# Optimization experiments

Measured on AMD Instinct MI355X. Metric: run time of the kernel, lower is better.

The kernel has to match this reference:

```python
import jax, jax.numpy as jnp
import numpy as np

B, Q, S, D, H, F = 16, 8, 4096, 2048, 16, 128  # batch, new tokens, past kv, d_state, heads, head_dim
W_SCALE = 0.02  # keep projections well-conditioned for stable softmax


def setup_inputs() -> dict:
    key = jax.random.key(0)
    ks = jax.random.split(key, 8)
    return {
        "x": jax.random.normal(ks[0], (B, Q, D), jnp.float32),
        "cache_k": jax.random.normal(ks[1], (B, S, H, F), jnp.float32),
        "cache_v": jax.random.normal(ks[2], (B, S, H, F), jnp.float32),
        "wq": jax.random.normal(ks[3], (D, H, F), jnp.float32) * W_SCALE,
        "bq": jnp.zeros((H, F), jnp.float32),
        "wk": jax.random.normal(ks[4], (D, H, F), jnp.float32) * W_SCALE,
        "bk": jnp.zeros((H, F), jnp.float32),
        "wv": jax.random.normal(ks[5], (D, H, F), jnp.float32) * W_SCALE,
        "bv": jnp.zeros((H, F), jnp.float32),
        "wo": jax.random.normal(ks[6], (H, F, D), jnp.float32) * W_SCALE,
        "bo": jnp.zeros((D,), jnp.float32),
    }


def reference(x, cache_k, cache_v, wq, bq, wk, bk, wv, bv, wo, bo):
    # QKV projections: DenseGeneral(features=(H, F), axis=-1)
    q = jnp.einsum("bqd,dhf->bqhf", x, wq) + bq          # [B,Q,H,F]
    k_new = jnp.einsum("bqd,dhf->bqhf", x, wk) + bk      # [B,Q,H,F]
    v_new = jnp.einsum("bqd,dhf->bqhf", x, wv) + bv
    # concat-based KV cache growth along the sequence axis (axis=1)
    k = jnp.concatenate([cache_k, k_new], axis=1)        # [B,S+Q,H,F]
    v = jnp.concatenate([cache_v, v_new], axis=1)
    # full dot-product attention over the whole cache (mask=None on decode path)
    scale = 1.0 / jnp.sqrt(jnp.asarray(F, q.dtype))
    scores = jnp.einsum("bqhf,bkhf->bhqk", q, k) * scale  # [B,H,Q,S+Q]
    probs = jax.nn.softmax(scores, axis=-1)
    attn = jnp.einsum("bhqk,bkhf->bhqf", probs, v)        # [B,H,Q,F]
    # output projection: DenseGeneral(features=D, axis=(-3,-1)) contracts (H, F)
    out = jnp.einsum("bhqf,hfd->bqd", attn, wo) + bo      # [B,Q,D]
    return (out, k, v)
```

## Files before the change

kernel.cpp:

```cpp
#include <hip/hip_runtime.h>
#include <hip/hip_bf16.h>

constexpr int Bc = 16;
constexpr int Qc = 8;
constexpr int Sc = 4096;
constexpr int Dc = 2048;
constexpr int Hc = 16;
constexpr int Fc = 128;
constexpr int SP = Sc + Qc;
constexpr int Mr = Bc * Qc;
constexpr int NCHUNK = 9;
constexpr int CHUNK = 512;
constexpr float SCALE = 0.08838834764831845f;
constexpr int GKS = 8;
constexpr int GKC = Dc / GKS;

typedef float floatx4 __attribute__((ext_vector_type(4)));

__device__ __forceinline__ float4 nt_load4(const float* p) {
    floatx4 r = __builtin_nontemporal_load(reinterpret_cast<const floatx4*>(p));
    return make_float4(r.x, r.y, r.z, r.w);
}
__device__ __forceinline__ void nt_store4(float* p, float4 v) {
    floatx4 r; r.x = v.x; r.y = v.y; r.z = v.z; r.w = v.w;
    __builtin_nontemporal_store(r, reinterpret_cast<floatx4*>(p));
}

__global__ __launch_bounds__(256)
void gemm_ksplit(const float* __restrict__ A, const float* __restrict__ W0,
                 const float* __restrict__ W1, const float* __restrict__ W2,
                 float* __restrict__ part)
{
    const int ntile = blockIdx.x;
    const int mat   = blockIdx.y;
    const int kz    = blockIdx.z;
    const float* __restrict__ W = (mat == 0) ? W0 : ((mat == 1) ? W1 : W2);
    const int t  = threadIdx.x;
    const int tx = t & 15, ty = t >> 4;
    const int r0 = ty * 8, c0 = tx * 8;
    const int ncol0 = ntile * 128;

    __shared__ float a_s[128][17];
    __shared__ float w_s[16][128];

    float acc[8][8] = {};

    const int kbase = kz * GKC;
    for (int k0 = kbase; k0 < kbase + GKC; k0 += 16) {
        {
            const int kk = t & 15, r = t >> 4;
            #pragma unroll
            for (int i = 0; i < 8; i++)
                a_s[r + i * 16][kk] = A[(size_t)(r + i * 16) * Dc + k0 + kk];
        }
        {
            const int nn = t & 127, ks_ = t >> 7;
            #pragma unroll
            for (int i = 0; i < 8; i++)
                w_s[ks_ + i * 2][nn] = W[(size_t)(k0 + ks_ + i * 2) * 2048 + ncol0 + nn];
        }
        __syncthreads();
        #pragma unroll
        for (int kk = 0; kk < 16; kk++) {
            float av[8], wv[8];
            #pragma unroll
            for (int i = 0; i < 8; i++) av[i] = a_s[r0 + i][kk];
            #pragma unroll
            for (int j = 0; j < 8; j++) wv[j] = w_s[kk][c0 + j];
            #pragma unroll
            for (int i = 0; i < 8; i++)
                #pragma unroll
                for (int j = 0; j < 8; j++)
                    acc[i][j] += av[i] * wv[j];
        }
        __syncthreads();
    }
    float* __restrict__ dst = part + (size_t)(mat * GKS + kz) * Mr * 2048;
    #pragma unroll
    for (int i = 0; i < 8; i++)
        #pragma unroll
        for (int j = 0; j < 8; j++)
            dst[(size_t)(r0 + i) * 2048 + ncol0 + c0 + j] = acc[i][j];
}

__global__ __launch_bounds__(256)
void reduce_qkv(const float* __restrict__ part, const float* __restrict__ bq,
                const float* __restrict__ bk, const float* __restrict__ bv,
                float* __restrict__ q_ws, float* __restrict__ out_k, float* __restrict__ out_v)
{
    const int mat = blockIdx.y;
    const int e = blockIdx.x * 256 + threadIdx.x;
    const int m = e >> 11, n = e & 2047;
    const float* __restrict__ p = part + (size_t)mat * GKS * (Mr * 2048);
    float s = 0.f;
    #pragma unroll
    for (int ks = 0; ks < GKS; ks++) s += p[(size_t)ks * (Mr * 2048) + e];
    const int b = m >> 3, qi = m & 7;
    if (mat == 0)      { s += bq[n]; q_ws[e] = s; }
    else if (mat == 1) { s += bk[n]; out_k[((size_t)(b * SP + Sc + qi)) * 2048 + n] = s; }
    else               { s += bv[n]; out_v[((size_t)(b * SP + Sc + qi)) * 2048 + n] = s; }
}

template<bool TAIL, int LEN>
__global__ __launch_bounds__(256, 3)
void attn_fused(const float* __restrict__ cache_k, const float* __restrict__ cache_v,
                const float* __restrict__ q_ws,
                float* __restrict__ out_k, float* __restrict__ out_v,
                float* __restrict__ part_acc, float* __restrict__ part_l)
{
    const int c = TAIL ? 8 : blockIdx.x;
    const int h = blockIdx.y;
    const int b = blockIdx.z;
    const int t = threadIdx.x;
    const int w = t >> 6;
    const int lane = t & 63;
    const int half = lane >> 5;
    const int fl = lane & 31;
    const int s0 = c * CHUNK;

    constexpr int kpw = LEN / 4;
    constexpr int pairs = LEN / 8;

    __shared__ float wacc[4][Qc][Fc];
    __shared__ float l_w[4][Qc];

    float4 qreg[Qc];
    #pragma unroll
    for (int qi = 0; qi < Qc; qi++) {
        float4 qv = *reinterpret_cast<const float4*>(
            &q_ws[((size_t)(b * Qc + qi)) * Dc + h * Fc + fl * 4]);
        qv.x *= SCALE; qv.y *= SCALE; qv.z *= SCALE; qv.w *= SCALE;
        qreg[qi] = qv;
    }

    float4 acc[Qc];
    float lsum[Qc];
    #pragma unroll
    for (int i = 0; i < Qc; i++) { acc[i] = make_float4(0, 0, 0, 0); lsum[i] = 0.f; }

    #pragma unroll 4
    for (int j = 0; j < pairs; j++) {
        const int kl = w * kpw + 2 * j + half;
        const int key = s0 + kl;
        const size_t outoff = (((size_t)b * SP + key) * Hc + h) * Fc + fl * 4;
        float4 kv, vv;
        if (!TAIL) {
            const size_t coff = (((size_t)b * Sc + key) * Hc + h) * Fc + fl * 4;
            kv = nt_load4(&cache_k[coff]);
            vv = nt_load4(&cache_v[coff]);
            nt_store4(&out_k[outoff], kv);
            nt_store4(&out_v[outoff], vv);
        } else {
            kv = *reinterpret_cast<const float4*>(&out_k[outoff]);
            vv = *reinterpret_cast<const float4*>(&out_v[outoff]);
        }
        #pragma unroll
        for (int qi = 0; qi < Qc; qi++) {
            float p = kv.x * qreg[qi].x + kv.y * qreg[qi].y
                    + kv.z * qreg[qi].z + kv.w * qreg[qi].w;
            p += __shfl_xor(p, 1, 64);
            p += __shfl_xor(p, 2, 64);
            p += __shfl_xor(p, 4, 64);
            p += __shfl_xor(p, 8, 64);
            p += __shfl_xor(p, 16, 64);
            p = __expf(p);
            lsum[qi] += p;
            acc[qi].x += p * vv.x; acc[qi].y += p * vv.y;
            acc[qi].z += p * vv.z; acc[qi].w += p * vv.w;
        }
    }

    #pragma unroll
    for (int qi = 0; qi < Qc; qi++) {
        acc[qi].x += __shfl_xor(acc[qi].x, 32, 64);
        acc[qi].y += __shfl_xor(acc[qi].y, 32, 64);
        acc[qi].z += __shfl_xor(acc[qi].z, 32, 64);
        acc[qi].w += __shfl_xor(acc[qi].w, 32, 64);
        lsum[qi]  += __shfl_xor(lsum[qi], 32, 64);
    }
    if (half == 0) {
        #pragma unroll
        for (int qi = 0; qi < Qc; qi++)
            *reinterpret_cast<float4*>(&wacc[w][qi][fl * 4]) = acc[qi];
    }
    if (lane == 0) {
        #pragma unroll
        for (int qi = 0; qi < Qc; qi++) l_w[w][qi] = lsum[qi];
    }
    __syncthreads();

    {
        const int qi = t >> 5, f4 = (t & 31) * 4;
        float4 s_ = make_float4(0, 0, 0, 0);
        #pragma unroll
        for (int ww = 0; ww < 4; ww++) {
            const float4 a = *reinterpret_cast<const float4*>(&wacc[ww][qi][f4]);
            s_.x += a.x; s_.y += a.y; s_.z += a.z; s_.w += a.w;
        }
        const size_t idx = (size_t)(b * Hc + h) * NCHUNK + c;
        *reinterpret_cast<float4*>(&part_acc[(idx * Qc + qi) * Fc + f4]) = s_;
        if ((t & 31) == 0)
            part_l[idx * Qc + qi] = l_w[0][qi] + l_w[1][qi] + l_w[2][qi] + l_w[3][qi];
    }
}

__global__ __launch_bounds__(256)
void attn_combine(const float* __restrict__ part_acc, const float* __restrict__ part_l,
                  float* __restrict__ attn_ws)
{
    const int bh = blockIdx.x;
    const int b = bh >> 4, h = bh & 15;
    const int t = threadIdx.x;
    const int qi = t >> 5, f4 = (t & 31) * 4;
    const size_t base = (size_t)bh * NCHUNK;

    float lg = 0.f;
    #pragma unroll
    for (int c = 0; c < NCHUNK; c++) lg += part_l[(base + c) * Qc + qi];
    float4 s_ = make_float4(0, 0, 0, 0);
    #pragma unroll
    for (int c = 0; c < NCHUNK; c++) {
        const float4 a = *reinterpret_cast<const float4*>(
            &part_acc[((base + c) * Qc + qi) * Fc + f4]);
        s_.x += a.x; s_.y += a.y; s_.z += a.z; s_.w += a.w;
    }
    const float inv = 1.0f / lg;
    const float4 o = make_float4(s_.x * inv, s_.y * inv, s_.z * inv, s_.w * inv);
    *reinterpret_cast<float4*>(&attn_ws[((size_t)(b * Qc + qi)) * Dc + h * Fc + f4]) = o;
}

__global__ __launch_bounds__(256)
void reduce_o(const float* __restrict__ part, const float* __restrict__ bo,
              float* __restrict__ out)
{
    const int e = blockIdx.x * 256 + threadIdx.x;
    const int n = e & 2047;
    float s = 0.f;
    #pragma unroll
    for (int ks = 0; ks < GKS; ks++) s += part[(size_t)ks * (Mr * 2048) + e];
    out[e] = s + bo[n];
}

extern "C" void kernel_launch(void* const* d_in, const int* in_sizes, int n_in,
                              void* d_out, int out_size, void* d_ws, size_t ws_size,
                              hipStream_t stream)
{
    (void)in_sizes; (void)n_in; (void)out_size; (void)ws_size;
    const float* x       = (const float*)d_in[0];
    const float* cache_k = (const float*)d_in[1];
    const float* cache_v = (const float*)d_in[2];
    const float* wq      = (const float*)d_in[3];
    const float* bq      = (const float*)d_in[4];
    const float* wk      = (const float*)d_in[5];
    const float* bk      = (const float*)d_in[6];
    const float* wv      = (const float*)d_in[7];
    const float* bv      = (const float*)d_in[8];
    const float* wo      = (const float*)d_in[9];
    const float* bo      = (const float*)d_in[10];

    float* out   = (float*)d_out;
    float* out_k = out + (size_t)Mr * Dc;
    float* out_v = out_k + (size_t)Bc * SP * Hc * Fc;

    float* ws       = (float*)d_ws;
    float* q_ws     = ws;
    float* attn_ws  = ws + 262144;
    float* part_l   = ws + 524288;
    float* part_acc = part_l + 18432;
    float* gemm_part = part_acc + 2359296;

    gemm_ksplit<<<dim3(16, 3, GKS), 256, 0, stream>>>(x, wq, wk, wv, gemm_part);
    reduce_qkv<<<dim3(1024, 3), 256, 0, stream>>>(gemm_part, bq, bk, bv, q_ws, out_k, out_v);
    attn_fused<false, CHUNK><<<dim3(8, Hc, Bc), 256, 0, stream>>>(
        cache_k, cache_v, q_ws, out_k, out_v, part_acc, part_l);
    attn_fused<true, 8><<<dim3(1, Hc, Bc), 256, 0, stream>>>(
        cache_k, cache_v, q_ws, out_k, out_v, part_acc, part_l);
    attn_combine<<<dim3(Bc * Hc), 256, 0, stream>>>(part_acc, part_l, attn_ws);
    gemm_ksplit<<<dim3(16, 1, GKS), 256, 0, stream>>>(attn_ws, wo, wo, wo, gemm_part);
    reduce_o<<<dim3(1024), 256, 0, stream>>>(gemm_part, bo, out);
}
```

Before: 537.0 us.

## Split attention into 256-key chunks, fold tail into last chunk, vectorize reductions

Halves the attention chunk size to 256 keys (16 chunks) and reorders the grid so heads vary fastest, which gives more blocks and raises the occupancy hint to 4. The separate tail launch is removed: the last chunk now also handles the 8 new tokens. The exponential uses exp2 with log2e folded into the query scale. The two bias-and-reduce kernels now work on float4, and part_acc reuses the gemm_part workspace. The cost is more partials for the combine step and a runtime branch inside the attention kernel.

```diff
diff --git a/kernel.cpp b/kernel.cpp
--- a/kernel.cpp
+++ b/kernel.cpp
@@ -9,9 +9,11 @@
 constexpr int Fc = 128;
 constexpr int SP = Sc + Qc;
 constexpr int Mr = Bc * Qc;
-constexpr int NCHUNK = 9;
-constexpr int CHUNK = 512;
+constexpr int CHUNK = 256;
+constexpr int NCHUNK = 16;
 constexpr float SCALE = 0.08838834764831845f;
+constexpr float LOG2E = 1.4426950408889634f;
+constexpr float QSCALE = SCALE * LOG2E;
 constexpr int GKS = 8;
 constexpr int GKC = Dc / GKS;
 
@@ -89,27 +91,40 @@
                 float* __restrict__ q_ws, float* __restrict__ out_k, float* __restrict__ out_v)
 {
     const int mat = blockIdx.y;
-    const int e = blockIdx.x * 256 + threadIdx.x;
+    const int e4 = blockIdx.x * 256 + threadIdx.x;
+    const int e = e4 * 4;
     const int m = e >> 11, n = e & 2047;
     const float* __restrict__ p = part + (size_t)mat * GKS * (Mr * 2048);
-    float s = 0.f;
-    #pragma unroll
-    for (int ks = 0; ks < GKS; ks++) s += p[(size_t)ks * (Mr * 2048) + e];
+    float4 s = make_float4(0, 0, 0, 0);
+    #pragma unroll
+    for (int ks = 0; ks < GKS; ks++) {
+        const float4 a = *reinterpret_cast<const float4*>(&p[(size_t)ks * (Mr * 2048) + e]);
+        s.x += a.x; s.y += a.y; s.z += a.z; s.w += a.w;
+    }
     const int b = m >> 3, qi = m & 7;
-    if (mat == 0)      { s += bq[n]; q_ws[e] = s; }
-    else if (mat == 1) { s += bk[n]; out_k[((size_t)(b * SP + Sc + qi)) * 2048 + n] = s; }
-    else               { s += bv[n]; out_v[((size_t)(b * SP + Sc + qi)) * 2048 + n] = s; }
-}
-
-template<bool TAIL, int LEN>
-__global__ __launch_bounds__(256, 3)
+    if (mat == 0) {
+        const float4 bb = *reinterpret_cast<const float4*>(&bq[n]);
+        s.x += bb.x; s.y += bb.y; s.z += bb.z; s.w += bb.w;
+        *reinterpret_cast<float4*>(&q_ws[e]) = s;
+    } else if (mat == 1) {
+        const float4 bb = *reinterpret_cast<const float4*>(&bk[n]);
+        s.x += bb.x; s.y += bb.y; s.z += bb.z; s.w += bb.w;
+        *reinterpret_cast<float4*>(&out_k[((size_t)(b * SP + Sc + qi)) * 2048 + n]) = s;
+    } else {
+        const float4 bb = *reinterpret_cast<const float4*>(&bv[n]);
+        s.x += bb.x; s.y += bb.y; s.z += bb.z; s.w += bb.w;
+        *reinterpret_cast<float4*>(&out_v[((size_t)(b * SP + Sc + qi)) * 2048 + n]) = s;
+    }
+}
+
+__global__ __launch_bounds__(256, 4)
 void attn_fused(const float* __restrict__ cache_k, const float* __restrict__ cache_v,
                 const float* __restrict__ q_ws,
                 float* __restrict__ out_k, float* __restrict__ out_v,
                 float* __restrict__ part_acc, float* __restrict__ part_l)
 {
-    const int c = TAIL ? 8 : blockIdx.x;
-    const int h = blockIdx.y;
+    const int h = blockIdx.x;
+    const int c = blockIdx.y;
     const int b = blockIdx.z;
     const int t = threadIdx.x;
     const int w = t >> 6;
@@ -117,9 +132,10 @@
     const int half = lane >> 5;
     const int fl = lane & 31;
     const int s0 = c * CHUNK;
-
-    constexpr int kpw = LEN / 4;
-    constexpr int pairs = LEN / 8;
+    const bool tail = (c == NCHUNK - 1);
+    const int len = tail ? (CHUNK + Qc) : CHUNK;
+    const int kpw = len / 4;
+    const int pairs = len / 8;
 
     __shared__ float wacc[4][Qc][Fc];
     __shared__ float l_w[4][Qc];
@@ -129,7 +145,7 @@
     for (int qi = 0; qi < Qc; qi++) {
         float4 qv = *reinterpret_cast<const float4*>(
             &q_ws[((size_t)(b * Qc + qi)) * Dc + h * Fc + fl * 4]);
-        qv.x *= SCALE; qv.y *= SCALE; qv.z *= SCALE; qv.w *= SCALE;
+        qv.x *= QSCALE; qv.y *= QSCALE; qv.z *= QSCALE; qv.w *= QSCALE;
         qreg[qi] = qv;
     }
 
@@ -138,35 +154,63 @@
     #pragma unroll
     for (int i = 0; i < Qc; i++) { acc[i] = make_float4(0, 0, 0, 0); lsum[i] = 0.f; }
 
-    #pragma unroll 4
-    for (int j = 0; j < pairs; j++) {
-        const int kl = w * kpw + 2 * j + half;
-        const int key = s0 + kl;
-        const size_t outoff = (((size_t)b * SP + key) * Hc + h) * Fc + fl * 4;
-        float4 kv, vv;
-        if (!TAIL) {
+    if (!tail) {
+        #pragma unroll 4
+        for (int j = 0; j < CHUNK / 8; j++) {
+            const int kl = w * (CHUNK / 4) + 2 * j + half;
+            const int key = s0 + kl;
+            const size_t outoff = (((size_t)b * SP + key) * Hc + h) * Fc + fl * 4;
             const size_t coff = (((size_t)b * Sc + key) * Hc + h) * Fc + fl * 4;
-            kv = nt_load4(&cache_k[coff]);
-            vv = nt_load4(&cache_v[coff]);
+            const float4 kv = nt_load4(&cache_k[coff]);
+            const float4 vv = nt_load4(&cache_v[coff]);
             nt_store4(&out_k[outoff], kv);
             nt_store4(&out_v[outoff], vv);
-        } else {
-            kv = *reinterpret_cast<const float4*>(&out_k[outoff]);
-            vv = *reinterpret_cast<const float4*>(&out_v[outoff]);
-        }
-        #pragma unroll
-        for (int qi = 0; qi < Qc; qi++) {
-            float p = kv.x * qreg[qi].x + kv.y * qreg[qi].y
-                    + kv.z * qreg[qi].z + kv.w * qreg[qi].w;
-            p += __shfl_xor(p, 1, 64);
-            p += __shfl_xor(p, 2, 64);
-            p += __shfl_xor(p, 4, 64);
-            p += __shfl_xor(p, 8, 64);
-            p += __shfl_xor(p, 16, 64);
-            p = __expf(p);
-            lsum[qi] += p;
-            acc[qi].x += p * vv.x; acc[qi].y += p * vv.y;
-            acc[qi].z += p * vv.z; acc[qi].w += p * vv.w;
+            #pragma unroll
+            for (int qi = 0; qi < Qc; qi++) {
+                float p = kv.x * qreg[qi].x + kv.y * qreg[qi].y
+                        + kv.z * qreg[qi].z + kv.w * qreg[qi].w;
+                p += __shfl_xor(p, 1, 64);
+                p += __shfl_xor(p, 2, 64);
+                p += __shfl_xor(p, 4, 64);
+                p += __shfl_xor(p, 8, 64);
+                p += __shfl_xor(p, 16, 64);
+                p = __builtin_amdgcn_exp2f(p);
+                lsum[qi] += p;
+                acc[qi].x += p * vv.x; acc[qi].y += p * vv.y;
+                acc[qi].z += p * vv.z; acc[qi].w += p * vv.w;
+            }
+        }
+    } else {
+        #pragma unroll 4
+        for (int j = 0; j < (CHUNK + Qc) / 8; j++) {
+            const int kl = w * kpw + 2 * j + half;
+            const int key = s0 + kl;
+            const size_t outoff = (((size_t)b * SP + key) * Hc + h) * Fc + fl * 4;
+            float4 kv, vv;
+            if (key < Sc) {
+                const size_t coff = (((size_t)b * Sc + key) * Hc + h) * Fc + fl * 4;
+                kv = nt_load4(&cache_k[coff]);
+                vv = nt_load4(&cache_v[coff]);
+                nt_store4(&out_k[outoff], kv);
+                nt_store4(&out_v[outoff], vv);
+            } else {
+                kv = *reinterpret_cast<const float4*>(&out_k[outoff]);
+                vv = *reinterpret_cast<const float4*>(&out_v[outoff]);
+            }
+            #pragma unroll
+            for (int qi = 0; qi < Qc; qi++) {
+                float p = kv.x * qreg[qi].x + kv.y * qreg[qi].y
+                        + kv.z * qreg[qi].z + kv.w * qreg[qi].w;
+                p += __shfl_xor(p, 1, 64);
+                p += __shfl_xor(p, 2, 64);
+                p += __shfl_xor(p, 4, 64);
+                p += __shfl_xor(p, 8, 64);
+                p += __shfl_xor(p, 16, 64);
+                p = __builtin_amdgcn_exp2f(p);
+                lsum[qi] += p;
+                acc[qi].x += p * vv.x; acc[qi].y += p * vv.y;
+                acc[qi].z += p * vv.z; acc[qi].w += p * vv.w;
+            }
         }
     }
 
@@ -233,12 +277,18 @@
 void reduce_o(const float* __restrict__ part, const float* __restrict__ bo,
               float* __restrict__ out)
 {
-    const int e = blockIdx.x * 256 + threadIdx.x;
+    const int e4 = blockIdx.x * 256 + threadIdx.x;
+    const int e = e4 * 4;
     const int n = e & 2047;
-    float s = 0.f;
-    #pragma unroll
-    for (int ks = 0; ks < GKS; ks++) s += part[(size_t)ks * (Mr * 2048) + e];
-    out[e] = s + bo[n];
+    float4 s = make_float4(0, 0, 0, 0);
+    #pragma unroll
+    for (int ks = 0; ks < GKS; ks++) {
+        const float4 a = *reinterpret_cast<const float4*>(&part[(size_t)ks * (Mr * 2048) + e]);
+        s.x += a.x; s.y += a.y; s.z += a.z; s.w += a.w;
+    }
+    const float4 bb = *reinterpret_cast<const float4*>(&bo[n]);
+    s.x += bb.x; s.y += bb.y; s.z += bb.z; s.w += bb.w;
+    *reinterpret_cast<float4*>(&out[e]) = s;
 }
 
 extern "C" void kernel_launch(void* const* d_in, const int* in_sizes, int n_in,
@@ -266,16 +316,14 @@
     float* q_ws     = ws;
     float* attn_ws  = ws + 262144;
     float* part_l   = ws + 524288;
-    float* part_acc = part_l + 18432;
-    float* gemm_part = part_acc + 2359296;
+    float* gemm_part = ws + 557056;
+    float* part_acc = gemm_part;
 
     gemm_ksplit<<<dim3(16, 3, GKS), 256, 0, stream>>>(x, wq, wk, wv, gemm_part);
-    reduce_qkv<<<dim3(1024, 3), 256, 0, stream>>>(gemm_part, bq, bk, bv, q_ws, out_k, out_v);
-    attn_fused<false, CHUNK><<<dim3(8, Hc, Bc), 256, 0, stream>>>(
-        cache_k, cache_v, q_ws, out_k, out_v, part_acc, part_l);
-    attn_fused<true, 8><<<dim3(1, Hc, Bc), 256, 0, stream>>>(
+    reduce_qkv<<<dim3(256, 3), 256, 0, stream>>>(gemm_part, bq, bk, bv, q_ws, out_k, out_v);
+    attn_fused<<<dim3(Hc, NCHUNK, Bc), 256, 0, stream>>>(
         cache_k, cache_v, q_ws, out_k, out_v, part_acc, part_l);
     attn_combine<<<dim3(Bc * Hc), 256, 0, stream>>>(part_acc, part_l, attn_ws);
     gemm_ksplit<<<dim3(16, 1, GKS), 256, 0, stream>>>(attn_ws, wo, wo, wo, gemm_part);
-    reduce_o<<<dim3(1024), 256, 0, stream>>>(gemm_part, bo, out);
-}
+    reduce_o<<<dim3(256), 256, 0, stream>>>(gemm_part, bo, out);
+}
```

Result: slower. 657.0 us (+22.3%).
